# Kernel optimization log

Hardware: AMD Instinct MI355X
Metric: run time of the kernel (lower is better)

The kernel has to match this reference:

```python
import jax, jax.numpy as jnp
import numpy as np

NUM_EXPERTS = 64
TOP_K = 2


def setup_inputs() -> dict:
    key = jax.random.key(0)
    k1, k2 = jax.random.split(key)
    # [batch, seq_len, d_model] token activations
    x = jax.random.normal(k1, (4, 4096, 2048), dtype=jnp.float32)
    # router_dense weight (no bias): [d_model, num_experts]
    W = jax.random.normal(k2, (2048, NUM_EXPERTS), dtype=jnp.float32) * 0.02
    return {"x": x, "W": W}


def reference(x, W):
    # router logits: [B, S, E]
    router_logits = jnp.einsum("bsd,de->bse", x, W)
    # softmax router (router_type == 'softmax')
    router_probs = jax.nn.softmax(router_logits, axis=-1)
    # top-k expert selection per token (sorted=False in TF; value set identical)
    top_k_probs, top_k_indices = jax.lax.top_k(router_probs, TOP_K)
    # dispatch tensor: sum of one-hots == tensor_scatter_nd_add of ones -> [B, S, E]
    dispatch_tensor = jax.nn.one_hot(top_k_indices, NUM_EXPERTS, dtype=router_probs.dtype).sum(axis=-2)
    return dispatch_tensor, router_probs, top_k_probs, top_k_indices
```

## Files before the change

kernel.cpp:

```cpp
#include <hip/hip_runtime.h>

#define TTOT 16384
#define DDIM 2048
#define NEXP 64
#define TPB  32
#define KCH  256
#define NKS  8
#define WTERM (NEXP * DDIM)

typedef __attribute__((ext_vector_type(8))) short bf16x8;
typedef __attribute__((ext_vector_type(4))) float f32x4;
typedef __attribute__((ext_vector_type(4))) unsigned int u32x4;

__device__ __forceinline__ void split3(const f32x4 va, const f32x4 vb,
                                       bf16x8& h, bf16x8& m, bf16x8& l)
{
    const float f[8] = {va.x, va.y, va.z, va.w, vb.x, vb.y, vb.z, vb.w};
    unsigned int hu[8], mu[8], lu[8];
#pragma unroll
    for (int j = 0; j < 8; ++j) {
        const unsigned int xb = __float_as_uint(f[j]);
        const unsigned int hb = xb & 0xffff0000u;
        const float r1 = f[j] - __uint_as_float(hb);
        const unsigned int mb = __float_as_uint(r1) & 0xffff0000u;
        const float r2 = r1 - __uint_as_float(mb);
        hu[j] = hb; mu[j] = mb; lu[j] = __float_as_uint(r2);
    }
    u32x4 hw, mw, lw;
#pragma unroll
    for (int w = 0; w < 4; ++w) {
        hw[w] = (hu[2 * w] >> 16) | (hu[2 * w + 1] & 0xffff0000u);
        mw[w] = (mu[2 * w] >> 16) | (mu[2 * w + 1] & 0xffff0000u);
        lw[w] = (lu[2 * w] >> 16) | (lu[2 * w + 1] & 0xffff0000u);
    }
    h = __builtin_bit_cast(bf16x8, hw);
    m = __builtin_bit_cast(bf16x8, mw);
    l = __builtin_bit_cast(bf16x8, lw);
}

__global__ __launch_bounds__(256)
void w_split(const float* __restrict__ W, unsigned short* __restrict__ W4)
{
    const int q = blockIdx.x * 256 + threadIdx.x;
    const int e = q >> 11;
    const int d = q & 2047;
    const float w = W[(size_t)d * NEXP + e];
    const unsigned int xb = __float_as_uint(w);
    const unsigned int hb = xb & 0xffff0000u;
    const float r1 = w - __uint_as_float(hb);
    const unsigned int mb = __float_as_uint(r1) & 0xffff0000u;
    const float r2 = r1 - __uint_as_float(mb);
    const unsigned int lb = __float_as_uint(r2);
    const size_t o = ((size_t)(d >> 3) * 64 + e) * 8 + (d & 7);
    W4[o]             = (unsigned short)(hb >> 16);
    W4[o + WTERM]     = (unsigned short)(mb >> 16);
    W4[o + 2 * WTERM] = (unsigned short)(lb >> 16);
}

__global__ __launch_bounds__(512, 4)
void moe_gemm(const float* __restrict__ x, const unsigned short* __restrict__ W4,
              float* __restrict__ out)
{
    __shared__ float xs[2][8][32][32];
    __shared__ float L[TPB][NEXP + 1];
    const int tid  = threadIdx.x;
    const int lane = tid & 63;
    const int wq   = __builtin_amdgcn_readfirstlane(tid >> 6);
    const int lrow = lane & 15;
    const int lk   = lane >> 4;
    const int tokBase = blockIdx.x * TPB;
    const int kBase   = wq * KCH;

    f32x4 c[2][4];
#pragma unroll
    for (int mt = 0; mt < 2; ++mt)
#pragma unroll
        for (int nt = 0; nt < 4; ++nt)
            c[mt][nt] = (f32x4){0.0f, 0.0f, 0.0f, 0.0f};

    const int srow = lane >> 3;
    const int scol = (lane & 7) ^ srow;
    const float* sBase = x + (size_t)(tokBase + srow) * DDIM + kBase + scol * 4;

#define STAGE(ksn, dstbuf)                                                     \
    {                                                                          \
        const float* g_ = sBase + (ksn) * 32;                                  \
        float* l_ = &xs[dstbuf][wq][0][0];                                     \
        _Pragma("unroll")                                                      \
        for (int cc = 0; cc < 4; ++cc)                                         \
            __builtin_amdgcn_global_load_lds(                                  \
                (const __attribute__((address_space(1))) unsigned int*)        \
                    (g_ + cc * 8 * DDIM),                                      \
                (__attribute__((address_space(3))) unsigned int*)              \
                    (l_ + cc * 256),                                           \
                16, 0, 0);                                                     \
    }

    const int ph    = (lk * 2) ^ (lrow & 7);
    const int aoff0 = lrow * 32 + ph * 4;
    const int aoff1 = (16 + lrow) * 32 + ph * 4;

    const unsigned short* bph = W4 + (size_t)(((kBase >> 3) + lk) * 512 + lrow * 8);
    const unsigned short* bpm = bph + WTERM;
    const unsigned short* bpl = bpm + WTERM;

    STAGE(0, 0)

#pragma unroll 2
    for (int ks = 0; ks < NKS; ++ks) {
        asm volatile("s_waitcnt vmcnt(0)" ::: "memory");
        const int buf = ks & 1;
        if (ks + 1 < NKS) STAGE(ks + 1, buf ^ 1)

        bf16x8 bh[4], bm[4], bl[4];
#pragma unroll
        for (int nt = 0; nt < 4; ++nt) {
            bh[nt] = *(const bf16x8*)(bph + nt * 128);
            bm[nt] = *(const bf16x8*)(bpm + nt * 128);
            bl[nt] = *(const bf16x8*)(bpl + nt * 128);
        }
        bph += 2048; bpm += 2048; bpl += 2048;

        const float* sub = &xs[buf][wq][0][0];
        const f32x4 c0a = *(const f32x4*)(sub + aoff0);
        const f32x4 c0b = *(const f32x4*)(sub + (aoff0 ^ 4));
        const f32x4 c1a = *(const f32x4*)(sub + aoff1);
        const f32x4 c1b = *(const f32x4*)(sub + (aoff1 ^ 4));
        bf16x8 ah0, am0, al0, ah1, am1, al1;
        split3(c0a, c0b, ah0, am0, al0);
        split3(c1a, c1b, ah1, am1, al1);

#pragma unroll
        for (int nt = 0; nt < 4; ++nt) c[0][nt] = __builtin_amdgcn_mfma_f32_16x16x32_bf16(ah0, bh[nt], c[0][nt], 0, 0, 0);
#pragma unroll
        for (int nt = 0; nt < 4; ++nt) c[1][nt] = __builtin_amdgcn_mfma_f32_16x16x32_bf16(ah1, bh[nt], c[1][nt], 0, 0, 0);
#pragma unroll
        for (int nt = 0; nt < 4; ++nt) c[0][nt] = __builtin_amdgcn_mfma_f32_16x16x32_bf16(ah0, bm[nt], c[0][nt], 0, 0, 0);
#pragma unroll
        for (int nt = 0; nt < 4; ++nt) c[1][nt] = __builtin_amdgcn_mfma_f32_16x16x32_bf16(ah1, bm[nt], c[1][nt], 0, 0, 0);
#pragma unroll
        for (int nt = 0; nt < 4; ++nt) c[0][nt] = __builtin_amdgcn_mfma_f32_16x16x32_bf16(am0, bh[nt], c[0][nt], 0, 0, 0);
#pragma unroll
        for (int nt = 0; nt < 4; ++nt) c[1][nt] = __builtin_amdgcn_mfma_f32_16x16x32_bf16(am1, bh[nt], c[1][nt], 0, 0, 0);
#pragma unroll
        for (int nt = 0; nt < 4; ++nt) c[0][nt] = __builtin_amdgcn_mfma_f32_16x16x32_bf16(ah0, bl[nt], c[0][nt], 0, 0, 0);
#pragma unroll
        for (int nt = 0; nt < 4; ++nt) c[1][nt] = __builtin_amdgcn_mfma_f32_16x16x32_bf16(ah1, bl[nt], c[1][nt], 0, 0, 0);
#pragma unroll
        for (int nt = 0; nt < 4; ++nt) c[0][nt] = __builtin_amdgcn_mfma_f32_16x16x32_bf16(al0, bh[nt], c[0][nt], 0, 0, 0);
#pragma unroll
        for (int nt = 0; nt < 4; ++nt) c[1][nt] = __builtin_amdgcn_mfma_f32_16x16x32_bf16(al1, bh[nt], c[1][nt], 0, 0, 0);
#pragma unroll
        for (int nt = 0; nt < 4; ++nt) c[0][nt] = __builtin_amdgcn_mfma_f32_16x16x32_bf16(am0, bm[nt], c[0][nt], 0, 0, 0);
#pragma unroll
        for (int nt = 0; nt < 4; ++nt) c[1][nt] = __builtin_amdgcn_mfma_f32_16x16x32_bf16(am1, bm[nt], c[1][nt], 0, 0, 0);
    }
#undef STAGE

    for (int w = 0; w < 8; ++w) {
        if (wq == w) {
#pragma unroll
            for (int mt = 0; mt < 2; ++mt)
#pragma unroll
                for (int nt = 0; nt < 4; ++nt)
#pragma unroll
                    for (int i = 0; i < 4; ++i) {
                        const int row = mt * 16 + lk * 4 + i;
                        const int col = nt * 16 + lrow;
                        if (w == 0) L[row][col]  = c[mt][nt][i];
                        else        L[row][col] += c[mt][nt][i];
                    }
        }
        __syncthreads();
    }

    float* dispatch = out;
    float* probs    = out + (size_t)TTOT * NEXP;
    float* tkp      = out + (size_t)2 * TTOT * NEXP;
    float* tki      = tkp + (size_t)TTOT * 2;

#pragma unroll
    for (int tt = 0; tt < 4; ++tt) {
        const int te = wq * 4 + tt;
        const int gt = tokBase + te;
        const float Lg = L[te][lane];

        float m = Lg;
#pragma unroll
        for (int off = 32; off; off >>= 1) m = fmaxf(m, __shfl_xor(m, off, 64));
        const float p = expf(Lg - m);
        float sden = p;
#pragma unroll
        for (int off = 32; off; off >>= 1) sden += __shfl_xor(sden, off, 64);
        const float prob = p / sden;

        float v1 = prob; int i1 = lane;
#pragma unroll
        for (int off = 32; off; off >>= 1) {
            const float ov = __shfl_xor(v1, off, 64);
            const int   oi = __shfl_xor(i1, off, 64);
            if (ov > v1 || (ov == v1 && oi < i1)) { v1 = ov; i1 = oi; }
        }
        float v2 = (lane == i1) ? -1.0f : prob; int i2 = lane;
#pragma unroll
        for (int off = 32; off; off >>= 1) {
            const float ov = __shfl_xor(v2, off, 64);
            const int   oi = __shfl_xor(i2, off, 64);
            if (ov > v2 || (ov == v2 && oi < i2)) { v2 = ov; i2 = oi; }
        }

        probs[(size_t)gt * NEXP + lane]    = prob;
        dispatch[(size_t)gt * NEXP + lane] = (lane == i1 || lane == i2) ? 1.0f : 0.0f;
        if (lane == 0) {
            tkp[(size_t)gt * 2 + 0] = v1;
            tkp[(size_t)gt * 2 + 1] = v2;
            tki[(size_t)gt * 2 + 0] = (float)i1;
            tki[(size_t)gt * 2 + 1] = (float)i2;
        }
    }
}

extern "C" void kernel_launch(void* const* d_in, const int* in_sizes, int n_in,
                              void* d_out, int out_size, void* d_ws, size_t ws_size,
                              hipStream_t stream) {
    const float* x = (const float*)d_in[0];
    const float* W = (const float*)d_in[1];
    float* out = (float*)d_out;
    unsigned short* W4 = (unsigned short*)d_ws;

    w_split<<<512, 256, 0, stream>>>(W, W4);
    moe_gemm<<<TTOT / TPB, 512, 0, stream>>>(x, W4, out);
}
```

Measured before the change: 215.1 us.

## Load x fragments directly into registers with two-deep prefetch, dropping LDS staging

Replaces the async global-to-LDS double-buffered staging of the activation tile with direct per-lane vector loads into registers, prefetched two k-steps ahead. This removes the LDS round trip, the 32 KB shared buffer and the full vmcnt(0) wait each iteration. In exchange, per-lane global loads are less coalesced (32-byte chunks per lane across 16 rows) and register pressure rises, which could hurt occupancy under the 512x4 launch bound.

```diff
diff --git a/kernel.cpp b/kernel.cpp
--- a/kernel.cpp
+++ b/kernel.cpp
@@ -61,7 +61,6 @@
 void moe_gemm(const float* __restrict__ x, const unsigned short* __restrict__ W4,
               float* __restrict__ out)
 {
-    __shared__ float xs[2][8][32][32];
     __shared__ float L[TPB][NEXP + 1];
     const int tid  = threadIdx.x;
     const int lane = tid & 63;
@@ -78,54 +77,43 @@
         for (int nt = 0; nt < 4; ++nt)
             c[mt][nt] = (f32x4){0.0f, 0.0f, 0.0f, 0.0f};
 
-    const int srow = lane >> 3;
-    const int scol = (lane & 7) ^ srow;
-    const float* sBase = x + (size_t)(tokBase + srow) * DDIM + kBase + scol * 4;
-
-#define STAGE(ksn, dstbuf)                                                     \
-    {                                                                          \
-        const float* g_ = sBase + (ksn) * 32;                                  \
-        float* l_ = &xs[dstbuf][wq][0][0];                                     \
-        _Pragma("unroll")                                                      \
-        for (int cc = 0; cc < 4; ++cc)                                         \
-            __builtin_amdgcn_global_load_lds(                                  \
-                (const __attribute__((address_space(1))) unsigned int*)        \
-                    (g_ + cc * 8 * DDIM),                                      \
-                (__attribute__((address_space(3))) unsigned int*)              \
-                    (l_ + cc * 256),                                           \
-                16, 0, 0);                                                     \
-    }
-
-    const int ph    = (lk * 2) ^ (lrow & 7);
-    const int aoff0 = lrow * 32 + ph * 4;
-    const int aoff1 = (16 + lrow) * 32 + ph * 4;
+    const float* xp0 = x + (size_t)(tokBase + lrow) * DDIM + kBase + lk * 8;
+    const float* xp1 = xp0 + (size_t)16 * DDIM;
 
     const unsigned short* bph = W4 + (size_t)(((kBase >> 3) + lk) * 512 + lrow * 8);
     const unsigned short* bpm = bph + WTERM;
     const unsigned short* bpl = bpm + WTERM;
 
-    STAGE(0, 0)
-
-#pragma unroll 2
+    f32x4 a0a[2], a0b[2], a1a[2], a1b[2];
+#pragma unroll
+    for (int p = 0; p < 2; ++p) {
+        a0a[p] = *(const f32x4*)(xp0 + p * 32);
+        a0b[p] = *(const f32x4*)(xp0 + p * 32 + 4);
+        a1a[p] = *(const f32x4*)(xp1 + p * 32);
+        a1b[p] = *(const f32x4*)(xp1 + p * 32 + 4);
+    }
+
+#pragma unroll
     for (int ks = 0; ks < NKS; ++ks) {
-        asm volatile("s_waitcnt vmcnt(0)" ::: "memory");
-        const int buf = ks & 1;
-        if (ks + 1 < NKS) STAGE(ks + 1, buf ^ 1)
+        const int p = ks & 1;
 
         bf16x8 bh[4], bm[4], bl[4];
 #pragma unroll
         for (int nt = 0; nt < 4; ++nt) {
-            bh[nt] = *(const bf16x8*)(bph + nt * 128);
-            bm[nt] = *(const bf16x8*)(bpm + nt * 128);
-            bl[nt] = *(const bf16x8*)(bpl + nt * 128);
-        }
-        bph += 2048; bpm += 2048; bpl += 2048;
-
-        const float* sub = &xs[buf][wq][0][0];
-        const f32x4 c0a = *(const f32x4*)(sub + aoff0);
-        const f32x4 c0b = *(const f32x4*)(sub + (aoff0 ^ 4));
-        const f32x4 c1a = *(const f32x4*)(sub + aoff1);
-        const f32x4 c1b = *(const f32x4*)(sub + (aoff1 ^ 4));
+            bh[nt] = *(const bf16x8*)(bph + ks * 2048 + nt * 128);
+            bm[nt] = *(const bf16x8*)(bpm + ks * 2048 + nt * 128);
+            bl[nt] = *(const bf16x8*)(bpl + ks * 2048 + nt * 128);
+        }
+
+        const f32x4 c0a = a0a[p], c0b = a0b[p];
+        const f32x4 c1a = a1a[p], c1b = a1b[p];
+        if (ks + 2 < NKS) {
+            a0a[p] = *(const f32x4*)(xp0 + (ks + 2) * 32);
+            a0b[p] = *(const f32x4*)(xp0 + (ks + 2) * 32 + 4);
+            a1a[p] = *(const f32x4*)(xp1 + (ks + 2) * 32);
+            a1b[p] = *(const f32x4*)(xp1 + (ks + 2) * 32 + 4);
+        }
+
         bf16x8 ah0, am0, al0, ah1, am1, al1;
         split3(c0a, c0b, ah0, am0, al0);
         split3(c1a, c1b, ah1, am1, al1);
@@ -155,7 +143,6 @@
 #pragma unroll
         for (int nt = 0; nt < 4; ++nt) c[1][nt] = __builtin_amdgcn_mfma_f32_16x16x32_bf16(am1, bm[nt], c[1][nt], 0, 0, 0);
     }
-#undef STAGE
 
     for (int w = 0; w < 8; ++w) {
         if (wq == w) {
```

New measurement: 231.1 us. 7.4% more time.

## Split-K GEMM with LDS-staged weights and separate softmax/top-k finish kernel

Applied to the files above, without the earlier changes.

Replaces the single fused kernel, where each block of 32 tokens splits K across 8 waves and reduces through LDS, with a 128-token by 4-way K-split GEMM. This kernel stages both x and the three bf16 weight terms into LDS through async global-to-LDS loads, so weight fragments are shared across waves instead of each wave reading them from global memory. Partial logits go to a workspace buffer, and a second kernel sums them and does softmax and top-2. This adds a 16 MB partial-logit round trip through memory and an extra launch, and it depends on the workspace being large enough, otherwise the old fused path runs.

```diff
diff --git a/kernel.cpp b/kernel.cpp
--- a/kernel.cpp
+++ b/kernel.cpp
@@ -3,10 +3,15 @@
 #define TTOT 16384
 #define DDIM 2048
 #define NEXP 64
+#define WTERM (NEXP * DDIM)
+
+#define MBLK 128
+#define KSPL 4
+#define KBLK (DDIM / KSPL)
+#define NKS6 (KBLK / 32)
 #define TPB  32
 #define KCH  256
 #define NKS  8
-#define WTERM (NEXP * DDIM)
 
 typedef __attribute__((ext_vector_type(8))) short bf16x8;
 typedef __attribute__((ext_vector_type(4))) float f32x4;
@@ -57,9 +62,206 @@
     W4[o + 2 * WTERM] = (unsigned short)(lb >> 16);
 }
 
+__global__ __launch_bounds__(256, 2)
+void moe_gemm6(const float* __restrict__ x, const unsigned short* __restrict__ W4,
+               float* __restrict__ pl)
+{
+    __shared__ float as[2][MBLK][32];
+    __shared__ __align__(16) unsigned char bs[2][3][4][1040];
+    const int tid  = threadIdx.x;
+    const int lane = tid & 63;
+    const int wq   = __builtin_amdgcn_readfirstlane(tid >> 6);
+    const int lrow = lane & 15;
+    const int lk   = lane >> 4;
+    const int kblk = blockIdx.x & 3;
+    const int mblk = blockIdx.x >> 2;
+    const int tokBase = mblk * MBLK;
+    const int kBase   = kblk * KBLK;
+
+    f32x4 c[2][4];
+#pragma unroll
+    for (int mt = 0; mt < 2; ++mt)
+#pragma unroll
+        for (int nt = 0; nt < 4; ++nt)
+            c[mt][nt] = (f32x4){0.0f, 0.0f, 0.0f, 0.0f};
+
+    const float* aSrc[4];
+    int aDstOff[4];
+#pragma unroll
+    for (int cc = 0; cc < 4; ++cc) {
+        const int gi = cc * 256 + tid;
+        const int t  = gi >> 3;
+        const int g  = (gi & 7) ^ (t & 7);
+        aSrc[cc]    = x + (size_t)(tokBase + t) * DDIM + kBase + g * 4;
+        aDstOff[cc] = gi * 16;
+    }
+    const unsigned short* bSrc[3];
+    int bDstOff[3];
+#pragma unroll
+    for (int cc = 0; cc < 3; ++cc) {
+        const int q2   = cc * 4 + wq;
+        const int term = q2 >> 2;
+        const int row  = q2 & 3;
+        bSrc[cc]    = W4 + (size_t)term * WTERM + ((kBase >> 3) + row) * 512 + lane * 8;
+        bDstOff[cc] = term * 4160 + row * 1040 + lane * 16;
+    }
+
+#define STAGE6(ksn, dbuf)                                                      \
+    {                                                                          \
+        unsigned char* aB = (unsigned char*)&as[dbuf][0][0];                   \
+        unsigned char* bB = &bs[dbuf][0][0][0];                                \
+        _Pragma("unroll")                                                      \
+        for (int cc = 0; cc < 4; ++cc)                                         \
+            __builtin_amdgcn_global_load_lds(                                  \
+                (const __attribute__((address_space(1))) unsigned int*)        \
+                    (aSrc[cc] + (ksn) * 32),                                   \
+                (__attribute__((address_space(3))) unsigned int*)              \
+                    (aB + aDstOff[cc]), 16, 0, 0);                             \
+        _Pragma("unroll")                                                      \
+        for (int cc = 0; cc < 3; ++cc)                                         \
+            __builtin_amdgcn_global_load_lds(                                  \
+                (const __attribute__((address_space(1))) unsigned int*)        \
+                    (bSrc[cc] + (ksn) * 2048),                                 \
+                (__attribute__((address_space(3))) unsigned int*)              \
+                    (bB + bDstOff[cc]), 16, 0, 0);                             \
+    }
+
+    const int t0 = wq * 32 + lrow;
+    const int t1 = t0 + 16;
+    const int q0 = (lk * 2) ^ (t0 & 7);
+    const int q1 = (lk * 2) ^ (t1 & 7);
+    const int aOff0 = t0 * 32 + q0 * 4;
+    const int aOff1 = t1 * 32 + q1 * 4;
+
+    STAGE6(0, 0)
+    __syncthreads();
+
+#pragma unroll 2
+    for (int ks = 0; ks < NKS6; ++ks) {
+        const int buf = ks & 1;
+        if (ks + 1 < NKS6) STAGE6(ks + 1, buf ^ 1)
+
+        const unsigned char* bb = &bs[buf][0][0][0];
+        bf16x8 bh[4], bm[4], bl[4];
+#pragma unroll
+        for (int nt = 0; nt < 4; ++nt) {
+            const int eo = (nt * 16 + lrow) * 16 + lk * 1040;
+            bh[nt] = *(const bf16x8*)(bb + eo);
+            bm[nt] = *(const bf16x8*)(bb + 4160 + eo);
+            bl[nt] = *(const bf16x8*)(bb + 8320 + eo);
+        }
+
+        const float* sub = &as[buf][0][0];
+        const f32x4 c0a = *(const f32x4*)(sub + aOff0);
+        const f32x4 c0b = *(const f32x4*)(sub + (aOff0 ^ 4));
+        const f32x4 c1a = *(const f32x4*)(sub + aOff1);
+        const f32x4 c1b = *(const f32x4*)(sub + (aOff1 ^ 4));
+        bf16x8 ah0, am0, al0, ah1, am1, al1;
+        split3(c0a, c0b, ah0, am0, al0);
+        split3(c1a, c1b, ah1, am1, al1);
+
+#pragma unroll
+        for (int nt = 0; nt < 4; ++nt) c[0][nt] = __builtin_amdgcn_mfma_f32_16x16x32_bf16(ah0, bh[nt], c[0][nt], 0, 0, 0);
+#pragma unroll
+        for (int nt = 0; nt < 4; ++nt) c[1][nt] = __builtin_amdgcn_mfma_f32_16x16x32_bf16(ah1, bh[nt], c[1][nt], 0, 0, 0);
+#pragma unroll
+        for (int nt = 0; nt < 4; ++nt) c[0][nt] = __builtin_amdgcn_mfma_f32_16x16x32_bf16(ah0, bm[nt], c[0][nt], 0, 0, 0);
+#pragma unroll
+        for (int nt = 0; nt < 4; ++nt) c[1][nt] = __builtin_amdgcn_mfma_f32_16x16x32_bf16(ah1, bm[nt], c[1][nt], 0, 0, 0);
+#pragma unroll
+        for (int nt = 0; nt < 4; ++nt) c[0][nt] = __builtin_amdgcn_mfma_f32_16x16x32_bf16(am0, bh[nt], c[0][nt], 0, 0, 0);
+#pragma unroll
+        for (int nt = 0; nt < 4; ++nt) c[1][nt] = __builtin_amdgcn_mfma_f32_16x16x32_bf16(am1, bh[nt], c[1][nt], 0, 0, 0);
+#pragma unroll
+        for (int nt = 0; nt < 4; ++nt) c[0][nt] = __builtin_amdgcn_mfma_f32_16x16x32_bf16(ah0, bl[nt], c[0][nt], 0, 0, 0);
+#pragma unroll
+        for (int nt = 0; nt < 4; ++nt) c[1][nt] = __builtin_amdgcn_mfma_f32_16x16x32_bf16(ah1, bl[nt], c[1][nt], 0, 0, 0);
+#pragma unroll
+        for (int nt = 0; nt < 4; ++nt) c[0][nt] = __builtin_amdgcn_mfma_f32_16x16x32_bf16(al0, bh[nt], c[0][nt], 0, 0, 0);
+#pragma unroll
+        for (int nt = 0; nt < 4; ++nt) c[1][nt] = __builtin_amdgcn_mfma_f32_16x16x32_bf16(al1, bh[nt], c[1][nt], 0, 0, 0);
+#pragma unroll
+        for (int nt = 0; nt < 4; ++nt) c[0][nt] = __builtin_amdgcn_mfma_f32_16x16x32_bf16(am0, bm[nt], c[0][nt], 0, 0, 0);
+#pragma unroll
+        for (int nt = 0; nt < 4; ++nt) c[1][nt] = __builtin_amdgcn_mfma_f32_16x16x32_bf16(am1, bm[nt], c[1][nt], 0, 0, 0);
+
+        __syncthreads();
+    }
+#undef STAGE6
+
+    float* plp = pl + (size_t)kblk * TTOT * NEXP;
+#pragma unroll
+    for (int mt = 0; mt < 2; ++mt)
+#pragma unroll
+        for (int nt = 0; nt < 4; ++nt)
+#pragma unroll
+            for (int i = 0; i < 4; ++i) {
+                const int row = tokBase + wq * 32 + mt * 16 + lk * 4 + i;
+                const int col = nt * 16 + lrow;
+                plp[(size_t)row * NEXP + col] = c[mt][nt][i];
+            }
+}
+
+__global__ __launch_bounds__(256)
+void moe_finish(const float* __restrict__ pl, float* __restrict__ out)
+{
+    const int tid  = threadIdx.x;
+    const int lane = tid & 63;
+    const int wq   = __builtin_amdgcn_readfirstlane(tid >> 6);
+    const int tokBase = blockIdx.x * 32;
+
+    float* dispatch = out;
+    float* probs    = out + (size_t)TTOT * NEXP;
+    float* tkp      = out + (size_t)2 * TTOT * NEXP;
+    float* tki      = tkp + (size_t)TTOT * 2;
+
+#pragma unroll
+    for (int tt = 0; tt < 8; ++tt) {
+        const int gt = tokBase + wq * 8 + tt;
+        const size_t o = (size_t)gt * NEXP + lane;
+        float Lg = pl[o];
+        Lg += pl[o + (size_t)TTOT * NEXP];
+        Lg += pl[o + (size_t)2 * TTOT * NEXP];
+        Lg += pl[o + (size_t)3 * TTOT * NEXP];
+
+        float m = Lg;
+#pragma unroll
+        for (int off = 32; off; off >>= 1) m = fmaxf(m, __shfl_xor(m, off, 64));
+        const float p = expf(Lg - m);
+        float sden = p;
+#pragma unroll
+        for (int off = 32; off; off >>= 1) sden += __shfl_xor(sden, off, 64);
+        const float prob = p / sden;
+
+        float v1 = prob; int i1 = lane;
+#pragma unroll
+        for (int off = 32; off; off >>= 1) {
+            const float ov = __shfl_xor(v1, off, 64);
+            const int   oi = __shfl_xor(i1, off, 64);
+            if (ov > v1 || (ov == v1 && oi < i1)) { v1 = ov; i1 = oi; }
+        }
+        float v2 = (lane == i1) ? -1.0f : prob; int i2 = lane;
+#pragma unroll
+        for (int off = 32; off; off >>= 1) {
+            const float ov = __shfl_xor(v2, off, 64);
+            const int   oi = __shfl_xor(i2, off, 64);
+            if (ov > v2 || (ov == v2 && oi < i2)) { v2 = ov; i2 = oi; }
+        }
+
+        probs[(size_t)gt * NEXP + lane]    = prob;
+        dispatch[(size_t)gt * NEXP + lane] = (lane == i1 || lane == i2) ? 1.0f : 0.0f;
+        if (lane == 0) {
+            tkp[(size_t)gt * 2 + 0] = v1;
+            tkp[(size_t)gt * 2 + 1] = v2;
+            tki[(size_t)gt * 2 + 0] = (float)i1;
+            tki[(size_t)gt * 2 + 1] = (float)i2;
+        }
+    }
+}
+
 __global__ __launch_bounds__(512, 4)
-void moe_gemm(const float* __restrict__ x, const unsigned short* __restrict__ W4,
-              float* __restrict__ out)
+void moe_gemm_fb(const float* __restrict__ x, const unsigned short* __restrict__ W4,
+                 float* __restrict__ out)
 {
     __shared__ float xs[2][8][32][32];
     __shared__ float L[TPB][NEXP + 1];
@@ -82,7 +284,7 @@
     const int scol = (lane & 7) ^ srow;
     const float* sBase = x + (size_t)(tokBase + srow) * DDIM + kBase + scol * 4;
 
-#define STAGE(ksn, dstbuf)                                                     \
+#define STAGEF(ksn, dstbuf)                                                    \
     {                                                                          \
         const float* g_ = sBase + (ksn) * 32;                                  \
         float* l_ = &xs[dstbuf][wq][0][0];                                     \
@@ -92,8 +294,7 @@
                 (const __attribute__((address_space(1))) unsigned int*)        \
                     (g_ + cc * 8 * DDIM),                                      \
                 (__attribute__((address_space(3))) unsigned int*)              \
-                    (l_ + cc * 256),                                           \
-                16, 0, 0);                                                     \
+                    (l_ + cc * 256), 16, 0, 0);                                \
     }
 
     const int ph    = (lk * 2) ^ (lrow & 7);
@@ -104,22 +305,21 @@
     const unsigned short* bpm = bph + WTERM;
     const unsigned short* bpl = bpm + WTERM;
 
-    STAGE(0, 0)
+    STAGEF(0, 0)
 
 #pragma unroll 2
     for (int ks = 0; ks < NKS; ++ks) {
         asm volatile("s_waitcnt vmcnt(0)" ::: "memory");
         const int buf = ks & 1;
-        if (ks + 1 < NKS) STAGE(ks + 1, buf ^ 1)
+        if (ks + 1 < NKS) STAGEF(ks + 1, buf ^ 1)
 
         bf16x8 bh[4], bm[4], bl[4];
 #pragma unroll
         for (int nt = 0; nt < 4; ++nt) {
-            bh[nt] = *(const bf16x8*)(bph + nt * 128);
-            bm[nt] = *(const bf16x8*)(bpm + nt * 128);
-            bl[nt] = *(const bf16x8*)(bpl + nt * 128);
-        }
-        bph += 2048; bpm += 2048; bpl += 2048;
+            bh[nt] = *(const bf16x8*)(bph + ks * 2048 + nt * 128);
+            bm[nt] = *(const bf16x8*)(bpm + ks * 2048 + nt * 128);
+            bl[nt] = *(const bf16x8*)(bpl + ks * 2048 + nt * 128);
+        }
 
         const float* sub = &xs[buf][wq][0][0];
         const f32x4 c0a = *(const f32x4*)(sub + aoff0);
@@ -155,7 +355,7 @@
 #pragma unroll
         for (int nt = 0; nt < 4; ++nt) c[1][nt] = __builtin_amdgcn_mfma_f32_16x16x32_bf16(am1, bm[nt], c[1][nt], 0, 0, 0);
     }
-#undef STAGE
+#undef STAGEF
 
     for (int w = 0; w < 8; ++w) {
         if (wq == w) {
@@ -229,5 +429,14 @@
     unsigned short* W4 = (unsigned short*)d_ws;
 
     w_split<<<512, 256, 0, stream>>>(W, W4);
-    moe_gemm<<<TTOT / TPB, 512, 0, stream>>>(x, W4, out);
-}
+
+    const size_t plOff  = 1u << 20;
+    const size_t plSize = (size_t)KSPL * TTOT * NEXP * 4;
+    if (ws_size >= plOff + plSize) {
+        float* pl = (float*)((char*)d_ws + plOff);
+        moe_gemm6<<<(TTOT / MBLK) * KSPL, 256, 0, stream>>>(x, W4, pl);
+        moe_finish<<<TTOT / 32, 256, 0, stream>>>(pl, out);
+    } else {
+        moe_gemm_fb<<<TTOT / TPB, 512, 0, stream>>>(x, W4, out);
+    }
+}
```

After: 217.7 us. Within noise of the previous version (+1.2%).
